# Performance work log

Measured on AMD Instinct MI355X. Metric: run time of the kernel, lower is better.

The kernel has to match this reference:

```python
import jax, jax.numpy as jnp
import numpy as np

E = 16777216       # total edges across the batch
NG = 1024          # num_graphs
K = 32             # action_topk
TEMP = 1.0         # policy_temperature


def setup_inputs() -> dict:
    key = jax.random.key(0)
    k1, k2, k3, k4, k5 = jax.random.split(key, 5)
    edge_logits = jax.random.normal(k1, (E,), dtype=jnp.float32)
    edge_scores = jax.random.normal(k2, (E,), dtype=jnp.float32)
    stop_logits = jax.random.normal(k3, (NG,), dtype=jnp.float32)
    edge_batch = jnp.sort(jax.random.randint(k4, (E,), 0, NG)).astype(jnp.int64)
    candidate_mask = jax.random.randint(k5, (E,), 0, 2).astype(bool)
    return {
        'edge_logits': edge_logits,
        'edge_scores': edge_scores,
        'stop_logits': stop_logits,
        'edge_batch': edge_batch,
        'candidate_mask': candidate_mask,
    }


def _topk_edge_mask(edge_scores, edge_batch, candidate_mask):
    """Faithful port of _select_topk_candidate_edges, returning a boolean keep
    mask over all E edges (fixed shape; indices of kept edges are implicit)."""
    neg_inf = jnp.finfo(jnp.float32).min
    # Non-candidates get a sentinel segment NG and -inf score so they sort last.
    seg_key = jnp.where(candidate_mask, edge_batch, NG)
    score = jnp.where(candidate_mask, edge_scores.astype(jnp.float32), neg_inf)
    # Sort by score descending, then stable-sort by segment id
    order_score = jnp.argsort(-score)
    seg_by_score = seg_key[order_score]
    order_seg = jnp.argsort(seg_by_score)          # jax argsort is stable
    cand_sorted = order_score[order_seg]           # original edge ids, sorted
    seg_sorted = seg_by_score[order_seg]
    # rank within each segment = position - segment start (exclusive cumsum)
    counts = jnp.bincount(seg_sorted, length=NG + 1)
    start = jnp.concatenate([jnp.zeros((1,), counts.dtype), jnp.cumsum(counts)[:-1]])
    rank = jnp.arange(E) - start[seg_sorted]
    keep_sorted = (rank < K) & (seg_sorted < NG)
    return jnp.zeros((E,), dtype=bool).at[cand_sorted].set(keep_sorted)


def _segment_logsumexp_1d(logits, segment_ids, num_segments):
    """Faithful port of torch _segment_logsumexp_1d."""
    neg_inf = jnp.finfo(logits.dtype).min
    eps = jnp.finfo(logits.dtype).eps
    max_per = jnp.full((num_segments,), neg_inf, dtype=logits.dtype).at[segment_ids].max(logits)
    exp = jnp.exp(logits - max_per[segment_ids])
    sum_per = jnp.zeros((num_segments,), dtype=logits.dtype).at[segment_ids].add(exp)
    return jnp.log(jnp.maximum(sum_per, eps)) + max_per


def reference(edge_logits, edge_scores, stop_logits, edge_batch, candidate_mask):
    neg_inf = jnp.finfo(jnp.float32).min
    # Per-graph top-k pruning of candidate edges by edge_scores
    valid = _topk_edge_mask(edge_scores, edge_batch, candidate_mask)
    # Segmented temperature softmax over (valid edges + stop action)
    logits_t = edge_logits / TEMP
    stop_t = stop_logits / TEMP
    masked = jnp.where(valid, logits_t, neg_inf)
    lse_edges = _segment_logsumexp_1d(masked, edge_batch, NG)       # [NG]
    log_denom = jnp.logaddexp(lse_edges, stop_t)                    # [NG]
    log_prob_edge = jnp.where(valid, logits_t - log_denom[edge_batch], neg_inf)
    return log_prob_edge
```

## Files before the change

kernel.cpp:

```cpp
#include <hip/hip_runtime.h>
#include <float.h>

#define TPB  512
#define FTPB 256
#define KTOP 32
#define GCAP 512
#define LCAP 1024
#define SENT_U32 0xFF7F0000u
#define VCLAMP 3.0e38f
#define STHRESH 2.0f

__device__ __forceinline__ unsigned int f2u(float f){
  unsigned int u = __float_as_uint(f);
  return (u & 0x80000000u) ? ~u : (u | 0x80000000u);
}

__global__ void __launch_bounds__(FTPB, 8)
k_fill(float* __restrict__ out, int E)
{
  const float SENT = __uint_as_float(SENT_U32);
  const float4 sv = make_float4(SENT, SENT, SENT, SENT);
  float4* out4 = (float4*)out;
  int n4 = E >> 2;
  int stride = gridDim.x * blockDim.x;
  for (int q = blockIdx.x * blockDim.x + threadIdx.x; q < n4; q += stride)
    out4[q] = sv;
  for (int i = (n4 << 2) + blockIdx.x * blockDim.x + threadIdx.x; i < E; i += stride)
    out[i] = SENT;
}

__device__ int suffix_total(int* hist, int NB, int* gsum, int tid){
  int GS = NB >> 8;
  if (tid < 256){
    int p = 0, base = tid * GS;
    for (int j = 0; j < GS; ++j) p += hist[base + j];
    gsum[tid] = p;
  }
  __syncthreads();
  for (int d = 1; d < 256; d <<= 1){
    int v = 0;
    if (tid < 256) v = (tid + d < 256) ? gsum[tid + d] : 0;
    __syncthreads();
    if (tid < 256) gsum[tid] += v;
    __syncthreads();
  }
  return gsum[0];
}

__device__ int find_bin(int* hist, int NB, int* gsum, int R, int* s2, int tid,
                        int* above_out){
  int GS = NB >> 8;
  if (tid < 256){
    int St  = gsum[tid];
    int St1 = (tid < 255) ? gsum[tid + 1] : 0;
    if (R > St1 && R <= St) s2[0] = tid;
  }
  __syncthreads();
  if (tid == 0){
    int G = s2[0];
    int above = (G < 255) ? gsum[G + 1] : 0;
    int b = (G + 1) * GS - 1;
    for (; b > G * GS; --b){
      int h = hist[b];
      if (above + h >= R) break;
      above += h;
    }
    s2[0] = b; s2[1] = above;
  }
  __syncthreads();
  int bin = s2[0];
  *above_out = s2[1];
  __syncthreads();
  return bin;
}

__global__ void __launch_bounds__(TPB, 4)
k_select(const float* __restrict__ logits,
         const float* __restrict__ scores,
         const float* __restrict__ stop_logits,
         const int* __restrict__ batch,
         const int* __restrict__ cmask,
         float* __restrict__ out, int E, int NG)
{
  __shared__ int hist[2048];
  __shared__ int gsum[256];
  __shared__ int s2[2];
  __shared__ int sbounds[2];
  __shared__ int srch[2];
  __shared__ unsigned int st_u[LCAP];
  __shared__ int st_i[LCAP];
  __shared__ unsigned int bin_u[GCAP];
  __shared__ int bin_i[GCAP];
  __shared__ int ab_i[KTOP];
  __shared__ int vidx[KTOP];
  __shared__ float vlog[KTOP];
  __shared__ int scnt, cnt_bin, cnt_ab, vcnt;
  __shared__ float sh_logden;

  int tid = threadIdx.x;
  int g = blockIdx.x;

  {
    int grp = tid >> 8 & 1;
    int lt  = tid & 255;
    int target = g + grp;
    int lo = 0, hi = E;
    for (int round = 0; round < 3; ++round){
      if (lt == 0) srch[grp] = 0;
      __syncthreads();
      int width = hi - lo;
      int pred = 0;
      if (width > 256){
        long long w = width;
        int q = lo + (int)((w * (long long)lt) >> 8);
        pred = (batch[q] < target) ? 1 : 0;
      }
      unsigned long long bal = __ballot(pred);
      if ((tid & 63) == 0) atomicAdd(&srch[grp], __popcll(bal));
      __syncthreads();
      if (width > 256){
        long long w = width;
        int c = srch[grp];
        int nlo = (c > 0)   ? lo + (int)((w * (long long)(c - 1)) >> 8) + 1 : lo;
        int nhi = (c < 256) ? lo + (int)((w * (long long)c) >> 8)          : hi;
        lo = nlo; hi = nhi;
      }
      __syncthreads();
    }
    if (lt == 0) srch[grp] = 0;
    __syncthreads();
    int width = hi - lo;
    int pred = (lt < width) ? ((batch[lo + lt] < target) ? 1 : 0) : 0;
    unsigned long long bal = __ballot(pred);
    if ((tid & 63) == 0) atomicAdd(&srch[grp], __popcll(bal));
    __syncthreads();
    if (lt == 0) sbounds[grp] = lo + srch[grp];
  }
  if (tid == 0){ scnt = 0; cnt_bin = 0; cnt_ab = 0; vcnt = 0; }
  __syncthreads();
  int s = sbounds[0], e = sbounds[1];

  int s4 = (s + 3) & ~3; if (s4 > e) s4 = e;
  int e4 = e & ~3;       if (e4 < s4) e4 = s4;
  const float4* sc4 = (const float4*)scores;

  auto proc4 = [&](float4 a, int bidx){
    int h = (a.x >= STHRESH ? 1 : 0) | (a.y >= STHRESH ? 2 : 0)
          | (a.z >= STHRESH ? 4 : 0) | (a.w >= STHRESH ? 8 : 0);
    if (h){
      int sl = atomicAdd(&scnt, __popc(h));
      if (h & 1){ if (sl < LCAP){ st_u[sl] = f2u(a.x); st_i[sl] = bidx;     } sl++; }
      if (h & 2){ if (sl < LCAP){ st_u[sl] = f2u(a.y); st_i[sl] = bidx + 1; } sl++; }
      if (h & 4){ if (sl < LCAP){ st_u[sl] = f2u(a.z); st_i[sl] = bidx + 2; } sl++; }
      if (h & 8){ if (sl < LCAP){ st_u[sl] = f2u(a.w); st_i[sl] = bidx + 3; } }
    }
  };
  auto st1 = [&](float sc, int idx){
    if (sc >= STHRESH){
      int sl = atomicAdd(&scnt, 1);
      if (sl < LCAP){ st_u[sl] = f2u(sc); st_i[sl] = idx; }
    }
  };
  {
    int i = s + tid;  if (i < s4) st1(scores[i], i);
    int j = e4 + tid; if (j < e)  st1(scores[j], j);
    int q  = (s4 >> 2) + tid;
    int qe = (e4 >> 2);
    for (; q + 3 * TPB < qe; q += 4 * TPB){
      float4 a0 = sc4[q];
      float4 a1 = sc4[q +     TPB];
      float4 a2 = sc4[q + 2 * TPB];
      float4 a3 = sc4[q + 3 * TPB];
      proc4(a0, q << 2);
      proc4(a1, (q +     TPB) << 2);
      proc4(a2, (q + 2 * TPB) << 2);
      proc4(a3, (q + 3 * TPB) << 2);
    }
    for (; q < qe; q += TPB){
      float4 a = sc4[q];
      proc4(a, q << 2);
    }
  }
  __syncthreads();

  int nst = scnt;
  bool ovf = (nst > LCAP);
  if (!ovf){
    for (int t = tid; t < nst; t += TPB){
      int idx = st_i[t];
      if (cmask[idx]){
        int sl = atomicAdd(&cnt_bin, 1);
        if (sl < GCAP){ bin_u[sl] = st_u[t]; bin_i[sl] = idx; }
      }
    }
  }
  __syncthreads();
  int S = cnt_bin;

  if (!ovf && S >= KTOP && S <= GCAP){
    for (int jj = tid; jj < S; jj += TPB){
      unsigned long long kj = ((unsigned long long)bin_u[jj] << 32)
                            | (unsigned long long)(unsigned)(~(unsigned)bin_i[jj]);
      int rank = 0;
      for (int k = 0; k < S; ++k){
        unsigned long long kk = ((unsigned long long)bin_u[k] << 32)
                              | (unsigned long long)(unsigned)(~(unsigned)bin_i[k]);
        rank += (kk > kj) ? 1 : 0;
      }
      if (rank < KTOP){
        int sl = atomicAdd(&vcnt, 1);
        if (sl < KTOP) vidx[sl] = bin_i[jj];
      }
    }
  } else {
    auto scan_sc = [&](auto&& fn){
      int i = s + tid;  if (i < s4) fn(scores[i], i);
      int j = e4 + tid; if (j < e)  fn(scores[j], j);
      for (int q = (s4 >> 2) + tid, qe = (e4 >> 2); q < qe; q += TPB){
        float4 sc = sc4[q];
        int base = q << 2;
        fn(sc.x, base);     fn(sc.y, base + 1);
        fn(sc.z, base + 2); fn(sc.w, base + 3);
      }
    };
    auto is_cand = [&](int idx) -> bool { return cmask[idx] != 0; };

    for (int b = tid; b < 2048; b += TPB) hist[b] = 0;
    if (tid == 0){ cnt_bin = 0; cnt_ab = 0; }
    __syncthreads();
    scan_sc([&](float sc, int idx){
      if (is_cand(idx)) atomicAdd(&hist[f2u(sc) >> 21], 1);
    });
    __syncthreads();
    int T = suffix_total(hist, 2048, gsum, tid);
    bool sel = (T > KTOP);
    unsigned int prefix = 0; int pshift = 32; int R = KTOP;
    if (sel){
      int above;
      int b1 = find_bin(hist, 2048, gsum, R, s2, tid, &above);
      R -= above; prefix = (unsigned)b1; pshift = 21;
      int hcnt = hist[b1];
      __syncthreads();
      if (hcnt > GCAP){
        for (int b = tid; b < 2048; b += TPB) hist[b] = 0;
        __syncthreads();
        scan_sc([&](float sc, int idx){
          unsigned u = f2u(sc);
          if ((u >> 21) == prefix && is_cand(idx))
            atomicAdd(&hist[(u >> 10) & 0x7FFu], 1);
        });
        __syncthreads();
        suffix_total(hist, 2048, gsum, tid);
        int b2 = find_bin(hist, 2048, gsum, R, s2, tid, &above);
        R -= above; prefix = (prefix << 11) | (unsigned)b2; pshift = 10;
        hcnt = hist[b2];
        __syncthreads();
        if (hcnt > GCAP){
          for (int b = tid; b < 1024; b += TPB) hist[b] = 0;
          __syncthreads();
          scan_sc([&](float sc, int idx){
            unsigned u = f2u(sc);
            if ((u >> 10) == prefix && is_cand(idx))
              atomicAdd(&hist[u & 0x3FFu], 1);
          });
          __syncthreads();
          suffix_total(hist, 1024, gsum, tid);
          int b3 = find_bin(hist, 1024, gsum, R, s2, tid, &above);
          R -= above; prefix = (prefix << 10) | (unsigned)b3; pshift = 0;
          __syncthreads();
        }
      }
      scan_sc([&](float sc, int idx){
        unsigned u = f2u(sc);
        unsigned hp = (pshift < 32) ? (u >> pshift) : 0u;
        if (hp >= prefix){
          if (is_cand(idx)){
            if (hp == prefix){
              int sl = atomicAdd(&cnt_bin, 1);
              if (sl < GCAP){ bin_u[sl] = u; bin_i[sl] = idx; }
            } else {
              int sl = atomicAdd(&cnt_ab, 1);
              if (sl < KTOP) ab_i[sl] = idx;
            }
          }
        }
      });
      __syncthreads();
      int bn = min(cnt_bin, GCAP);
      for (int jj = tid; jj < bn; jj += TPB){
        unsigned long long kj = ((unsigned long long)bin_u[jj] << 32)
                              | (unsigned long long)(unsigned)(~(unsigned)bin_i[jj]);
        int rank = 0;
        for (int k = 0; k < bn; ++k){
          unsigned long long kk2 = ((unsigned long long)bin_u[k] << 32)
                                 | (unsigned long long)(unsigned)(~(unsigned)bin_i[k]);
          rank += (kk2 > kj) ? 1 : 0;
        }
        if (rank < R){
          int sl = atomicAdd(&vcnt, 1);
          if (sl < KTOP) vidx[sl] = bin_i[jj];
        }
      }
      int na = min(cnt_ab, KTOP);
      for (int jj = tid; jj < na; jj += TPB){
        int sl = atomicAdd(&vcnt, 1);
        if (sl < KTOP) vidx[sl] = ab_i[jj];
      }
    } else {
      scan_sc([&](float sc, int idx){
        (void)sc;
        if (is_cand(idx)){
          int sl = atomicAdd(&vcnt, 1);
          if (sl < KTOP) vidx[sl] = idx;
        }
      });
    }
  }
  __syncthreads();

  int c = min(vcnt, KTOP);
  if (tid < c) vlog[tid] = logits[vidx[tid]];
  __syncthreads();
  if (tid < 64){
    float v = (tid < c) ? vlog[tid] : -FLT_MAX;
    float m = v;
    #pragma unroll
    for (int d = 32; d; d >>= 1) m = fmaxf(m, __shfl_xor(m, d));
    float ex = (tid < c) ? expf(v - m) : 0.f;
    #pragma unroll
    for (int d = 32; d; d >>= 1) ex += __shfl_xor(ex, d);
    if (tid == 0){
      float stop = stop_logits[g];
      float logden;
      if (c == 0){
        logden = stop;
      } else {
        float lse = logf(fmaxf(ex, FLT_EPSILON)) + m;
        float mx = fmaxf(lse, stop);
        float dd = fabsf(lse - stop);
        logden = mx + log1pf(expf(-dd));
      }
      sh_logden = logden;
    }
  }
  __syncthreads();

  if (tid < c){
    float val = vlog[tid] - sh_logden;
    if (!(val >= -VCLAMP)) val = -VCLAMP;
    if (val > VCLAMP)      val =  VCLAMP;
    out[vidx[tid]] = val;
  }
}

extern "C" void kernel_launch(void* const* d_in, const int* in_sizes, int n_in,
                              void* d_out, int out_size, void* d_ws, size_t ws_size,
                              hipStream_t stream){
  const float* edge_logits = (const float*)d_in[0];
  const float* edge_scores = (const float*)d_in[1];
  const float* stop_logits = (const float*)d_in[2];
  const int*   edge_batch  = (const int*)d_in[3];
  const int*   cmask       = (const int*)d_in[4];
  int E  = in_sizes[0];
  int NG = in_sizes[2];
  float* out = (float*)d_out;
  (void)d_ws; (void)ws_size;

  hipLaunchKernelGGL(k_fill, dim3(2048), dim3(FTPB), 0, stream, out, E);
  hipLaunchKernelGGL(k_select, dim3(NG), dim3(TPB), 0, stream,
                     edge_logits, edge_scores, stop_logits, edge_batch, cmask,
                     out, E, NG);
}
```

Measured before the change: 240.9 us.

## Split selection into scan, select and finish kernels using output as scratch

The single per-graph select kernel becomes three per-graph kernels. A 512-thread scan writes the above-threshold score candidates into each graph's own region of the output buffer. A lighter 256-thread select kernel reads them back, applies the candidate mask and ranks them, then writes the kept indices and values into the same region. A finish kernel fills each segment with the sentinel and scatters the kept values, replacing the global fill kernel. The aim is to shrink the heavy kernel's shared memory and threads for better occupancy and to fuse the sentinel fill per segment, at the cost of extra launches, repeated segment searches and round-trips through global memory. It also adds a one-wavefront fast path for tiny segments and relies on each segment being large enough to hold the scratch data.

Result: slower. 252.7 us (+4.9%).

```diff
diff --git a/kernel.cpp b/kernel.cpp
--- a/kernel.cpp
+++ b/kernel.cpp
@@ -1,32 +1,127 @@
 #include <hip/hip_runtime.h>
 #include <float.h>
 
-#define TPB  512
-#define FTPB 256
 #define KTOP 32
-#define GCAP 512
-#define LCAP 1024
+#define BCAP 512
 #define SENT_U32 0xFF7F0000u
 #define VCLAMP 3.0e38f
 #define STHRESH 2.0f
+#define OVERMARK 0x7FFFFFFF
 
 __device__ __forceinline__ unsigned int f2u(float f){
   unsigned int u = __float_as_uint(f);
   return (u & 0x80000000u) ? ~u : (u | 0x80000000u);
 }
 
-__global__ void __launch_bounds__(FTPB, 8)
-k_fill(float* __restrict__ out, int E)
+template<int LOG>
+__device__ void seg_bounds(const int* __restrict__ batch, int E, int g,
+                           int* srch, int* sbounds){
+  const int HALF = 1 << LOG;
+  int tid = threadIdx.x;
+  int grp = (tid >= HALF) ? 1 : 0;
+  int lt  = tid - grp * HALF;
+  int target = g + grp;
+  int lo = 0, hi = E;
+  for (int round = 0; round < 4; ++round){
+    if (lt == 0) srch[grp] = 0;
+    __syncthreads();
+    int width = hi - lo;
+    int pred = 0;
+    if (width > HALF){
+      long long w = width;
+      int q = lo + (int)((w * (long long)lt) >> LOG);
+      pred = (batch[q] < target) ? 1 : 0;
+    }
+    unsigned long long bal = __ballot(pred);
+    if ((tid & 63) == 0) atomicAdd(&srch[grp], __popcll(bal));
+    __syncthreads();
+    if (width > HALF){
+      long long w = width;
+      int c = srch[grp];
+      int nlo = (c > 0)    ? lo + (int)((w * (long long)(c - 1)) >> LOG) + 1 : lo;
+      int nhi = (c < HALF) ? lo + (int)((w * (long long)c) >> LOG)           : hi;
+      lo = nlo; hi = nhi;
+    }
+    __syncthreads();
+  }
+  if (lt == 0) srch[grp] = 0;
+  __syncthreads();
+  int width = hi - lo;
+  int pred = (lt < width) ? ((batch[lo + lt] < target) ? 1 : 0) : 0;
+  unsigned long long bal = __ballot(pred);
+  if ((tid & 63) == 0) atomicAdd(&srch[grp], __popcll(bal));
+  __syncthreads();
+  if (lt == 0) sbounds[grp] = lo + srch[grp];
+  __syncthreads();
+}
+
+__global__ void __launch_bounds__(512, 4)
+k_scan(const float* __restrict__ scores, const int* __restrict__ batch,
+       float* __restrict__ out, int E, int NG)
 {
-  const float SENT = __uint_as_float(SENT_U32);
-  const float4 sv = make_float4(SENT, SENT, SENT, SENT);
-  float4* out4 = (float4*)out;
-  int n4 = E >> 2;
-  int stride = gridDim.x * blockDim.x;
-  for (int q = blockIdx.x * blockDim.x + threadIdx.x; q < n4; q += stride)
-    out4[q] = sv;
-  for (int i = (n4 << 2) + blockIdx.x * blockDim.x + threadIdx.x; i < E; i += stride)
-    out[i] = SENT;
+  __shared__ unsigned int st_u[BCAP];
+  __shared__ int st_i[BCAP];
+  __shared__ int srch[2], sbounds[2];
+  __shared__ int scnt;
+  int tid = threadIdx.x, g = blockIdx.x;
+  if (tid == 0) scnt = 0;
+  seg_bounds<8>(batch, E, g, srch, sbounds);
+  int s = sbounds[0], e = sbounds[1];
+  if (e <= s) return;
+
+  int s4 = (s + 3) & ~3; if (s4 > e) s4 = e;
+  int e4 = e & ~3;       if (e4 < s4) e4 = s4;
+  const float4* sc4 = (const float4*)scores;
+
+  auto proc4 = [&](float4 a, int bidx){
+    int h = (a.x >= STHRESH ? 1 : 0) | (a.y >= STHRESH ? 2 : 0)
+          | (a.z >= STHRESH ? 4 : 0) | (a.w >= STHRESH ? 8 : 0);
+    if (h){
+      int sl = atomicAdd(&scnt, __popc(h));
+      if (h & 1){ if (sl < BCAP){ st_u[sl] = f2u(a.x); st_i[sl] = bidx;     } sl++; }
+      if (h & 2){ if (sl < BCAP){ st_u[sl] = f2u(a.y); st_i[sl] = bidx + 1; } sl++; }
+      if (h & 4){ if (sl < BCAP){ st_u[sl] = f2u(a.z); st_i[sl] = bidx + 2; } sl++; }
+      if (h & 8){ if (sl < BCAP){ st_u[sl] = f2u(a.w); st_i[sl] = bidx + 3; } }
+    }
+  };
+  auto st1 = [&](float sc, int idx){
+    if (sc >= STHRESH){
+      int sl = atomicAdd(&scnt, 1);
+      if (sl < BCAP){ st_u[sl] = f2u(sc); st_i[sl] = idx; }
+    }
+  };
+  {
+    int i = s + tid;  if (i < s4) st1(scores[i], i);
+    int j = e4 + tid; if (j < e)  st1(scores[j], j);
+    int q  = (s4 >> 2) + tid;
+    int qe = (e4 >> 2);
+    for (; q + 3 * 512 < qe; q += 4 * 512){
+      float4 a0 = sc4[q];
+      float4 a1 = sc4[q +     512];
+      float4 a2 = sc4[q + 2 * 512];
+      float4 a3 = sc4[q + 3 * 512];
+      proc4(a0, q << 2);
+      proc4(a1, (q +     512) << 2);
+      proc4(a2, (q + 2 * 512) << 2);
+      proc4(a3, (q + 3 * 512) << 2);
+    }
+    for (; q < qe; q += 512){
+      float4 a = sc4[q];
+      proc4(a, q << 2);
+    }
+  }
+  __syncthreads();
+  int n = scnt;
+  int cap = (e - s - 1) >> 1;
+  bool over = (n > BCAP) || (n > cap);
+  int* outw = (int*)out;
+  if (tid == 0) outw[s] = over ? OVERMARK : n;
+  if (!over){
+    for (int t = tid; t < n; t += 512){
+      outw[s + 1 + 2 * t] = (int)st_u[t];
+      outw[s + 2 + 2 * t] = st_i[t];
+    }
+  }
 }
 
 __device__ int suffix_total(int* hist, int NB, int* gsum, int tid){
@@ -74,7 +169,7 @@
   return bin;
 }
 
-__global__ void __launch_bounds__(TPB, 4)
+__global__ void __launch_bounds__(256)
 k_select(const float* __restrict__ logits,
          const float* __restrict__ scores,
          const float* __restrict__ stop_logits,
@@ -82,141 +177,122 @@
          const int* __restrict__ cmask,
          float* __restrict__ out, int E, int NG)
 {
+  __shared__ unsigned int bin_u[BCAP];
+  __shared__ int          bin_i[BCAP];
+  __shared__ unsigned int sv_u[BCAP];
+  __shared__ int          sv_i[BCAP];
   __shared__ int hist[2048];
   __shared__ int gsum[256];
   __shared__ int s2[2];
-  __shared__ int sbounds[2];
-  __shared__ int srch[2];
-  __shared__ unsigned int st_u[LCAP];
-  __shared__ int st_i[LCAP];
-  __shared__ unsigned int bin_u[GCAP];
-  __shared__ int bin_i[GCAP];
+  __shared__ int srch[2], sbounds[2];
   __shared__ int ab_i[KTOP];
   __shared__ int vidx[KTOP];
   __shared__ float vlog[KTOP];
-  __shared__ int scnt, cnt_bin, cnt_ab, vcnt;
+  __shared__ int cnt2, fcnt, cnt_ab, vcnt;
   __shared__ float sh_logden;
 
-  int tid = threadIdx.x;
-  int g = blockIdx.x;
-
-  {
-    int grp = tid >> 8 & 1;
-    int lt  = tid & 255;
-    int target = g + grp;
-    int lo = 0, hi = E;
-    for (int round = 0; round < 3; ++round){
-      if (lt == 0) srch[grp] = 0;
-      __syncthreads();
-      int width = hi - lo;
-      int pred = 0;
-      if (width > 256){
-        long long w = width;
-        int q = lo + (int)((w * (long long)lt) >> 8);
-        pred = (batch[q] < target) ? 1 : 0;
-      }
-      unsigned long long bal = __ballot(pred);
-      if ((tid & 63) == 0) atomicAdd(&srch[grp], __popcll(bal));
-      __syncthreads();
-      if (width > 256){
-        long long w = width;
-        int c = srch[grp];
-        int nlo = (c > 0)   ? lo + (int)((w * (long long)(c - 1)) >> 8) + 1 : lo;
-        int nhi = (c < 256) ? lo + (int)((w * (long long)c) >> 8)          : hi;
-        lo = nlo; hi = nhi;
-      }
-      __syncthreads();
-    }
-    if (lt == 0) srch[grp] = 0;
-    __syncthreads();
-    int width = hi - lo;
-    int pred = (lt < width) ? ((batch[lo + lt] < target) ? 1 : 0) : 0;
-    unsigned long long bal = __ballot(pred);
-    if ((tid & 63) == 0) atomicAdd(&srch[grp], __popcll(bal));
-    __syncthreads();
-    if (lt == 0) sbounds[grp] = lo + srch[grp];
-  }
-  if (tid == 0){ scnt = 0; cnt_bin = 0; cnt_ab = 0; vcnt = 0; }
-  __syncthreads();
-  int s = sbounds[0], e = sbounds[1];
-
-  int s4 = (s + 3) & ~3; if (s4 > e) s4 = e;
-  int e4 = e & ~3;       if (e4 < s4) e4 = s4;
+  int tid = threadIdx.x, g = blockIdx.x;
+  if (tid == 0){ cnt2 = 0; fcnt = 0; cnt_ab = 0; vcnt = 0; }
+  seg_bounds<7>(batch, E, g, srch, sbounds);
+  int s = sbounds[0], e = sbounds[1], len = e - s;
+  if (len == 0) return;
+  int* outw = (int*)out;
   const float4* sc4 = (const float4*)scores;
 
-  auto proc4 = [&](float4 a, int bidx){
-    int h = (a.x >= STHRESH ? 1 : 0) | (a.y >= STHRESH ? 2 : 0)
-          | (a.z >= STHRESH ? 4 : 0) | (a.w >= STHRESH ? 8 : 0);
-    if (h){
-      int sl = atomicAdd(&scnt, __popc(h));
-      if (h & 1){ if (sl < LCAP){ st_u[sl] = f2u(a.x); st_i[sl] = bidx;     } sl++; }
-      if (h & 2){ if (sl < LCAP){ st_u[sl] = f2u(a.y); st_i[sl] = bidx + 1; } sl++; }
-      if (h & 4){ if (sl < LCAP){ st_u[sl] = f2u(a.z); st_i[sl] = bidx + 2; } sl++; }
-      if (h & 8){ if (sl < LCAP){ st_u[sl] = f2u(a.w); st_i[sl] = bidx + 3; } }
-    }
-  };
-  auto st1 = [&](float sc, int idx){
-    if (sc >= STHRESH){
-      int sl = atomicAdd(&scnt, 1);
-      if (sl < LCAP){ st_u[sl] = f2u(sc); st_i[sl] = idx; }
-    }
-  };
-  {
-    int i = s + tid;  if (i < s4) st1(scores[i], i);
-    int j = e4 + tid; if (j < e)  st1(scores[j], j);
-    int q  = (s4 >> 2) + tid;
-    int qe = (e4 >> 2);
-    for (; q + 3 * TPB < qe; q += 4 * TPB){
-      float4 a0 = sc4[q];
-      float4 a1 = sc4[q +     TPB];
-      float4 a2 = sc4[q + 2 * TPB];
-      float4 a3 = sc4[q + 3 * TPB];
-      proc4(a0, q << 2);
-      proc4(a1, (q +     TPB) << 2);
-      proc4(a2, (q + 2 * TPB) << 2);
-      proc4(a3, (q + 3 * TPB) << 2);
-    }
-    for (; q < qe; q += TPB){
-      float4 a = sc4[q];
-      proc4(a, q << 2);
-    }
-  }
-  __syncthreads();
-
-  int nst = scnt;
-  bool ovf = (nst > LCAP);
-  if (!ovf){
-    for (int t = tid; t < nst; t += TPB){
-      int idx = st_i[t];
+  if (len < 2 * KTOP + 1){
+    if (tid < 64){
+      float sc = 0.f; int cm = 0; float lg = 0.f;
+      if (tid < len){ sc = scores[s + tid]; cm = cmask[s + tid]; lg = logits[s + tid]; }
+      bool cand = (tid < len) && (cm != 0);
+      unsigned key = cand ? f2u(sc) : 0u;
+      unsigned long long kj = ((unsigned long long)key << 32)
+                            | (unsigned)(~(unsigned)(s + tid));
+      int rank = 0;
+      for (int k = 0; k < 64; ++k){
+        unsigned ok = __shfl(key, k);
+        int oc = __shfl(cand ? 1 : 0, k);
+        unsigned long long kk = ((unsigned long long)ok << 32)
+                              | (unsigned)(~(unsigned)(s + k));
+        rank += (oc && kk > kj) ? 1 : 0;
+      }
+      bool valid = cand && (rank < KTOP);
+      float v = valid ? lg : -FLT_MAX;
+      float m = v;
+      #pragma unroll
+      for (int d = 32; d; d >>= 1) m = fmaxf(m, __shfl_xor(m, d));
+      float ex = valid ? expf(v - m) : 0.f;
+      #pragma unroll
+      for (int d = 32; d; d >>= 1) ex += __shfl_xor(ex, d);
+      unsigned long long vb = __ballot(valid);
+      float logden = 0.f;
+      if (tid == 0){
+        float stop = stop_logits[g];
+        if (vb == 0ull) logden = stop;
+        else {
+          float lse = logf(fmaxf(ex, FLT_EPSILON)) + m;
+          float mx = fmaxf(lse, stop);
+          float dd = fabsf(lse - stop);
+          logden = mx + log1pf(expf(-dd));
+        }
+      }
+      logden = __shfl(logden, 0);
+      if (tid < len){
+        float ov;
+        if (valid){
+          float val = lg - logden;
+          if (!(val >= -VCLAMP)) val = -VCLAMP;
+          if (val > VCLAMP)      val =  VCLAMP;
+          ov = val;
+        } else ov = __uint_as_float(SENT_U32);
+        out[s + tid] = ov;
+      }
+    }
+    return;
+  }
+
+  int n = outw[s];
+  bool over = ((unsigned)n > (unsigned)BCAP);
+  if (!over){
+    for (int t = tid; t < n; t += 256){
+      bin_u[t] = (unsigned)outw[s + 1 + 2 * t];
+      bin_i[t] = outw[s + 2 + 2 * t];
+    }
+  }
+  __syncthreads();
+  if (!over){
+    for (int t = tid; t < n; t += 256){
+      int idx = bin_i[t];
       if (cmask[idx]){
-        int sl = atomicAdd(&cnt_bin, 1);
-        if (sl < GCAP){ bin_u[sl] = st_u[t]; bin_i[sl] = idx; }
-      }
-    }
-  }
-  __syncthreads();
-  int S = cnt_bin;
-
-  if (!ovf && S >= KTOP && S <= GCAP){
-    for (int jj = tid; jj < S; jj += TPB){
-      unsigned long long kj = ((unsigned long long)bin_u[jj] << 32)
-                            | (unsigned long long)(unsigned)(~(unsigned)bin_i[jj]);
+        int sl = atomicAdd(&cnt2, 1);
+        sv_u[sl] = bin_u[t]; sv_i[sl] = idx;
+      }
+    }
+  }
+  __syncthreads();
+  int S = cnt2;
+
+  if (!over && S >= KTOP){
+    for (int jj = tid; jj < S; jj += 256){
+      unsigned long long kj = ((unsigned long long)sv_u[jj] << 32)
+                            | (unsigned long long)(unsigned)(~(unsigned)sv_i[jj]);
       int rank = 0;
       for (int k = 0; k < S; ++k){
-        unsigned long long kk = ((unsigned long long)bin_u[k] << 32)
-                              | (unsigned long long)(unsigned)(~(unsigned)bin_i[k]);
+        unsigned long long kk = ((unsigned long long)sv_u[k] << 32)
+                              | (unsigned long long)(unsigned)(~(unsigned)sv_i[k]);
         rank += (kk > kj) ? 1 : 0;
       }
       if (rank < KTOP){
         int sl = atomicAdd(&vcnt, 1);
-        if (sl < KTOP) vidx[sl] = bin_i[jj];
+        if (sl < KTOP) vidx[sl] = sv_i[jj];
       }
     }
   } else {
+    int s4 = (s + 3) & ~3; if (s4 > e) s4 = e;
+    int e4 = e & ~3;       if (e4 < s4) e4 = s4;
     auto scan_sc = [&](auto&& fn){
       int i = s + tid;  if (i < s4) fn(scores[i], i);
       int j = e4 + tid; if (j < e)  fn(scores[j], j);
-      for (int q = (s4 >> 2) + tid, qe = (e4 >> 2); q < qe; q += TPB){
+      for (int q = (s4 >> 2) + tid, qe = (e4 >> 2); q < qe; q += 256){
         float4 sc = sc4[q];
         int base = q << 2;
         fn(sc.x, base);     fn(sc.y, base + 1);
@@ -225,8 +301,8 @@
     };
     auto is_cand = [&](int idx) -> bool { return cmask[idx] != 0; };
 
-    for (int b = tid; b < 2048; b += TPB) hist[b] = 0;
-    if (tid == 0){ cnt_bin = 0; cnt_ab = 0; }
+    for (int b = tid; b < 2048; b += 256) hist[b] = 0;
+    if (tid == 0){ fcnt = 0; cnt_ab = 0; }
     __syncthreads();
     scan_sc([&](float sc, int idx){
       if (is_cand(idx)) atomicAdd(&hist[f2u(sc) >> 21], 1);
@@ -241,8 +317,8 @@
       R -= above; prefix = (unsigned)b1; pshift = 21;
       int hcnt = hist[b1];
       __syncthreads();
-      if (hcnt > GCAP){
-        for (int b = tid; b < 2048; b += TPB) hist[b] = 0;
+      if (hcnt > BCAP){
+        for (int b = tid; b < 2048; b += 256) hist[b] = 0;
         __syncthreads();
         scan_sc([&](float sc, int idx){
           unsigned u = f2u(sc);
@@ -255,8 +331,8 @@
         R -= above; prefix = (prefix << 11) | (unsigned)b2; pshift = 10;
         hcnt = hist[b2];
         __syncthreads();
-        if (hcnt > GCAP){
-          for (int b = tid; b < 1024; b += TPB) hist[b] = 0;
+        if (hcnt > BCAP){
+          for (int b = tid; b < 1024; b += 256) hist[b] = 0;
           __syncthreads();
           scan_sc([&](float sc, int idx){
             unsigned u = f2u(sc);
@@ -276,8 +352,8 @@
         if (hp >= prefix){
           if (is_cand(idx)){
             if (hp == prefix){
-              int sl = atomicAdd(&cnt_bin, 1);
-              if (sl < GCAP){ bin_u[sl] = u; bin_i[sl] = idx; }
+              int sl = atomicAdd(&fcnt, 1);
+              if (sl < BCAP){ bin_u[sl] = u; bin_i[sl] = idx; }
             } else {
               int sl = atomicAdd(&cnt_ab, 1);
               if (sl < KTOP) ab_i[sl] = idx;
@@ -286,8 +362,8 @@
         }
       });
       __syncthreads();
-      int bn = min(cnt_bin, GCAP);
-      for (int jj = tid; jj < bn; jj += TPB){
+      int bn = min(fcnt, BCAP);
+      for (int jj = tid; jj < bn; jj += 256){
         unsigned long long kj = ((unsigned long long)bin_u[jj] << 32)
                               | (unsigned long long)(unsigned)(~(unsigned)bin_i[jj]);
         int rank = 0;
@@ -302,7 +378,7 @@
         }
       }
       int na = min(cnt_ab, KTOP);
-      for (int jj = tid; jj < na; jj += TPB){
+      for (int jj = tid; jj < na; jj += 256){
         int sl = atomicAdd(&vcnt, 1);
         if (sl < KTOP) vidx[sl] = ab_i[jj];
       }
@@ -345,12 +421,45 @@
   }
   __syncthreads();
 
+  if (tid == 0) outw[s] = c;
   if (tid < c){
     float val = vlog[tid] - sh_logden;
     if (!(val >= -VCLAMP)) val = -VCLAMP;
     if (val > VCLAMP)      val =  VCLAMP;
-    out[vidx[tid]] = val;
-  }
+    outw[s + 1 + 2 * tid] = vidx[tid];
+    outw[s + 2 + 2 * tid] = __float_as_int(val);
+  }
+}
+
+__global__ void __launch_bounds__(256)
+k_finish(const int* __restrict__ batch, float* __restrict__ out, int E, int NG)
+{
+  __shared__ int srch[2], sbounds[2];
+  __shared__ int c_sh;
+  __shared__ int idxs[KTOP];
+  __shared__ int vals[KTOP];
+  int tid = threadIdx.x, g = blockIdx.x;
+  seg_bounds<7>(batch, E, g, srch, sbounds);
+  int s = sbounds[0], e = sbounds[1], len = e - s;
+  if (len < 2 * KTOP + 1) return;
+  int* outw = (int*)out;
+  if (tid == 0) c_sh = outw[s];
+  __syncthreads();
+  int c = c_sh; if (c < 0) c = 0; if (c > KTOP) c = KTOP;
+  if (tid < c){ idxs[tid] = outw[s + 1 + 2 * tid]; vals[tid] = outw[s + 2 + 2 * tid]; }
+  __syncthreads();
+
+  const float SENT = __uint_as_float(SENT_U32);
+  const float4 sv = make_float4(SENT, SENT, SENT, SENT);
+  float4* out4 = (float4*)out;
+  int s4 = (s + 3) & ~3; if (s4 > e) s4 = e;
+  int e4 = e & ~3;       if (e4 < s4) e4 = s4;
+  int i = s + tid;  if (i < s4) out[i] = SENT;
+  int j = e4 + tid; if (j < e)  out[j] = SENT;
+  for (int q = (s4 >> 2) + tid, qe = (e4 >> 2); q < qe; q += 256)
+    out4[q] = sv;
+  __syncthreads();
+  if (tid < c) out[idxs[tid]] = __int_as_float(vals[tid]);
 }
 
 extern "C" void kernel_launch(void* const* d_in, const int* in_sizes, int n_in,
@@ -366,8 +475,11 @@
   float* out = (float*)d_out;
   (void)d_ws; (void)ws_size;
 
-  hipLaunchKernelGGL(k_fill, dim3(2048), dim3(FTPB), 0, stream, out, E);
-  hipLaunchKernelGGL(k_select, dim3(NG), dim3(TPB), 0, stream,
+  hipLaunchKernelGGL(k_scan,   dim3(NG), dim3(512), 0, stream,
+                     edge_scores, edge_batch, out, E, NG);
+  hipLaunchKernelGGL(k_select, dim3(NG), dim3(256), 0, stream,
                      edge_logits, edge_scores, stop_logits, edge_batch, cmask,
                      out, E, NG);
-}
+  hipLaunchKernelGGL(k_finish, dim3(NG), dim3(256), 0, stream,
+                     edge_batch, out, E, NG);
+}
```
